# Optimization experiments

Measured on AMD Instinct MI355X. Metric: run time of the kernel, lower is better.

Reference implementation:

```python
import jax, jax.numpy as jnp
import numpy as np

R, N, E = 6, 50000, 200000
D, H, C, O = 768, 4, 64, 64  # input_dim, heads, hidden_dim1, output_dim


def _gatv2(x, src, tgt, Wl_r, Wr_r, att_r, b_r):
    # PyG GATv2Conv (concat=True, add_self_loops=True, negative_slope=0.2)
    n = x.shape[0]
    xl = (x @ Wl_r).reshape(n, H, C)  # source transform (lin_l)
    xr = (x @ Wr_r).reshape(n, H, C)  # target transform (lin_r)
    loops = jnp.arange(n, dtype=src.dtype)
    s = jnp.concatenate([src, loops])
    t = jnp.concatenate([tgt, loops])
    e = jax.nn.leaky_relu(xl[s] + xr[t], 0.2)          # [E+N, H, C]
    logits = jnp.einsum('ehc,hc->eh', e, att_r)         # [E+N, H]
    m = jax.ops.segment_max(logits, t, num_segments=n)  # softmax over incoming edges
    a = jnp.exp(logits - m[t])
    denom = jax.ops.segment_sum(a, t, num_segments=n)
    alpha = a / (denom[t] + 1e-16)
    msg = xl[s] * alpha[:, :, None]                     # [E+N, H, C]
    out = jax.ops.segment_sum(msg, t, num_segments=n)
    return out.reshape(n, H * C) + b_r


def _graphconv(x, src, tgt, W_rel, W_root, b):
    # PyG GraphConv (aggr='add'): lin_rel(sum_j x_j) + lin_root(x)
    agg = jax.ops.segment_sum(x[src], tgt, num_segments=x.shape[0])
    return agg @ W_rel + b + x @ W_root


def setup_inputs() -> dict:
    key = jax.random.key(0)
    ks = jax.random.split(key, 12)
    s = 0.05
    return {
        'x': jax.random.normal(ks[0], (N, D), jnp.float32),
        'edge_index': jax.random.randint(ks[1], (R, 2, E), 0, N, jnp.int32),
        'Wl': jax.random.normal(ks[2], (R, D, H * C), jnp.float32) * s,
        'Wr': jax.random.normal(ks[3], (R, D, H * C), jnp.float32) * s,
        'att': jax.random.normal(ks[4], (R, H, C), jnp.float32) * s,
        'b_gat': jax.random.normal(ks[5], (R, H * C), jnp.float32) * s,
        'W_rel1': jax.random.normal(ks[6], (R, H * C, C), jnp.float32) * s,
        'W_root1': jax.random.normal(ks[7], (R, H * C, C), jnp.float32) * s,
        'b1': jax.random.normal(ks[8], (R, C), jnp.float32) * s,
        'W_rel2': jax.random.normal(ks[9], (R, C, O), jnp.float32) * s,
        'W_root2': jax.random.normal(ks[10], (R, C, O), jnp.float32) * s,
        'b2': jax.random.normal(ks[11], (R, O), jnp.float32) * s,
    }


def reference(x, edge_index, Wl, Wr, att, b_gat, W_rel1, W_root1, b1, W_rel2, W_root2, b2):
    outs = []
    for r in range(R):  # fixed small set of structurally distinct relation towers
        src, tgt = edge_index[r, 0], edge_index[r, 1]
        h = _gatv2(x, src, tgt, Wl[r], Wr[r], att[r], b_gat[r])
        h = jax.nn.relu(h)
        h = jax.nn.relu(_graphconv(h, src, tgt, W_rel1[r], W_root1[r], b1[r]))
        h = _graphconv(h, src, tgt, W_rel2[r], W_root2[r], b2[r])
        outs.append(h)
    return jnp.stack(outs, axis=1)  # [N, R, O]
```

## Files before the change

kernel.cpp:

```cpp
#include <hip/hip_runtime.h>
#include <hip/hip_bf16.h>
#include <math.h>

#define RREL 6
#define NN   50000
#define EE   200000
#define DD   768
#define HH   4
#define CC   64
#define HC   256
#define OO   64
#define MPAD 50176
#define SCAN_B 49
#define NT   12

typedef __attribute__((ext_vector_type(8))) short short8;
typedef __attribute__((ext_vector_type(4))) float f32x4;
typedef __attribute__((ext_vector_type(8))) unsigned short ushort8v;
typedef __attribute__((ext_vector_type(4))) unsigned short ushort4v;

__device__ __forceinline__ float b2f(unsigned short u) {
  return __uint_as_float(((unsigned)u) << 16);
}
__device__ __forceinline__ unsigned short f2b(float f) {
  __hip_bfloat16 h = __float2bfloat16(f);
  unsigned short u;
  __builtin_memcpy(&u, &h, 2);
  return u;
}

__device__ __forceinline__ void gload16(const void* g, void* s) {
  typedef __attribute__((address_space(1))) void gvoid;
  typedef __attribute__((address_space(3))) void svoid;
  __builtin_amdgcn_global_load_lds((gvoid*)(unsigned long long)g,
                                   (svoid*)(unsigned long long)s, 16, 0, 0);
}

__global__ __launch_bounds__(256) void k_cvt_x(const float* __restrict__ x,
                                               unsigned short* __restrict__ xb) {
  long t = (long)blockIdx.x * 256 + threadIdx.x;
  long base = t * 8;
  int row = (int)(base / DD);
  ushort8v o;
  if (row < NN) {
    float4 a = *(const float4*)(x + base);
    float4 b = *(const float4*)(x + base + 4);
    o[0] = f2b(a.x); o[1] = f2b(a.y); o[2] = f2b(a.z); o[3] = f2b(a.w);
    o[4] = f2b(b.x); o[5] = f2b(b.y); o[6] = f2b(b.z); o[7] = f2b(b.w);
  } else {
    o = (ushort8v)0;
  }
  *(ushort8v*)(xb + base) = o;
}

__global__ __launch_bounds__(256) void k_repack_w(const float* __restrict__ Wl,
                                                  const float* __restrict__ Wr,
                                                  unsigned short* __restrict__ Wt) {
  __shared__ float t[32][33];
  int k0 = blockIdx.x * 32, j0 = blockIdx.y * 32, r = blockIdx.z;
  int tx = threadIdx.x & 31, ty = threadIdx.x >> 5;
#pragma unroll
  for (int s = 0; s < 4; s++) {
    int k = k0 + ty + 8 * s, j = j0 + tx;
    float v = (j < HC) ? Wl[((long)r * DD + k) * HC + j]
                       : Wr[((long)r * DD + k) * HC + (j - HC)];
    t[ty + 8 * s][tx] = v;
  }
  __syncthreads();
#pragma unroll
  for (int s = 0; s < 4; s++) {
    int j = j0 + ty + 8 * s, k = k0 + tx;
    Wt[((long)r * 512 + j) * DD + k] = f2b(t[tx][ty + 8 * s]);
  }
}

__global__ void k_repack_gc(const float* __restrict__ Wrel, const float* __restrict__ Wroot,
                            unsigned short* __restrict__ Bt, int K) {
  int idx = blockIdx.x * blockDim.x + threadIdx.x;
  if (idx >= RREL * 64 * K) return;
  int k = idx % K;
  int o = (idx / K) % 64;
  int r = idx / (64 * K);
  int h = K >> 1;
  float v = (k < h) ? Wrel[((long)r * h + k) * 64 + o]
                    : Wroot[((long)r * h + (k - h)) * 64 + o];
  Bt[idx] = f2b(v);
}

#define STAGE_A(HALF, TT)                                                              \
  if ((TT) < NT) {                                                                     \
    long ko = (long)(TT) * 128;                                                        \
    char* db = ldsA + (((TT) & 1) << 15);                                              \
    gload16(AgB + (long)((HALF) * 64 + rA) * 1536 + ko + xcol,                         \
            db + ((HALF) * 64) * 128 + wave * 1024);                                   \
    gload16(AgB + (long)((HALF) * 64 + 128 + rA) * 1536 + ko + xcol,                   \
            db + ((HALF) * 64 + 128) * 128 + wave * 1024);                             \
  }

#define STAGE_B(HALF, TT)                                                              \
  if ((TT) < NT) {                                                                     \
    long ko = (long)(TT) * 128;                                                        \
    char* db = ldsB + (((TT) & 1) << 15);                                              \
    gload16(BgB + (long)(rb0 + (HALF) * 32 + lane8) * 1536 + ko + xcol,                \
            db + (rb0 + (HALF) * 32) * 128);                                           \
    gload16(BgB + (long)(rb1 + (HALF) * 32 + lane8) * 1536 + ko + xcol,                \
            db + (rb1 + (HALF) * 32) * 128);                                           \
  }

#define MMQ(PA, AOFF, NH)                                                              \
  do {                                                                                 \
    _Pragma("unroll") for (int fi = 0; fi < 4; ++fi)                                   \
    _Pragma("unroll") for (int fj = 0; fj < 2; ++fj) {                                 \
      f32x4 c = acc[(AOFF) + fi][(NH) * 2 + fj];                                       \
      c = __builtin_amdgcn_mfma_f32_16x16x32_bf16(PA[fi][0], pb[NH][fj][0], c, 0, 0, 0);\
      c = __builtin_amdgcn_mfma_f32_16x16x32_bf16(PA[fi][1], pb[NH][fj][1], c, 0, 0, 0);\
      acc[(AOFF) + fi][(NH) * 2 + fj] = c;                                             \
    }                                                                                  \
  } while (0)

__global__ __launch_bounds__(512, 2) void k_gemm(const short* __restrict__ A,
                                                 const short* __restrict__ Bt,
                                                 unsigned short* __restrict__ Yall) {
  __shared__ __align__(16) char ldsA[65536];
  __shared__ __align__(16) char ldsB[65536];
  int tid = threadIdx.x;
  int wgid = blockIdx.x;
  int swz = (wgid & 7) * 294 + (wgid >> 3);
  int bm = swz / 12, bn = swz % 12;
  int lane = tid & 63, wave = tid >> 6;
  int warp_m = wave >> 2, warp_n = wave & 3;
  int wm = warp_m * 128, wn = warp_n * 64;
  int l16 = lane & 15, quad = lane >> 4;
  int gm0 = bm * 256;
  const char* AgB = (const char*)A + (long)gm0 * 1536;
  const char* BgB = (const char*)Bt + (long)bn * 256 * 1536;
  int rA = tid >> 3;
  int lane8 = lane >> 3;
  long xcol = (long)(((tid & 7) ^ (rA & 7)) * 16);
  int rb0 = (wave >> 2) * 64 + (wave & 3) * 8;
  int rb1 = rb0 + 128;
  int s0 = (quad ^ (l16 & 7)) * 16, s1 = s0 ^ 64;
  f32x4 acc[8][4] = {};

  STAGE_A(0, 0); STAGE_B(0, 0); STAGE_A(1, 0); STAGE_B(1, 0);
  STAGE_A(0, 1); STAGE_B(0, 1);
  asm volatile("s_waitcnt vmcnt(4)" ::: "memory");
  __builtin_amdgcn_s_barrier();

  for (int t = 0; t < NT; ++t) {
    int bo = (t & 1) << 15;
    const char* Ard = ldsA + bo + (wm + l16) * 128;
    const char* Brd = ldsB + bo + (wn + l16) * 128;
    short8 pa0[4][2], pa1[4][2], pb[2][2][2];
    STAGE_A(1, t + 1);
    STAGE_B(1, t + 1);
#pragma unroll
    for (int fi = 0; fi < 4; ++fi) {
      pa0[fi][0] = *(const short8*)(Ard + (fi * 16) * 128 + s0);
      pa0[fi][1] = *(const short8*)(Ard + (fi * 16) * 128 + s1);
    }
#pragma unroll
    for (int nh = 0; nh < 2; ++nh)
#pragma unroll
      for (int fj = 0; fj < 2; ++fj) {
        pb[nh][fj][0] = *(const short8*)(Brd + (nh * 32 + fj * 16) * 128 + s0);
        pb[nh][fj][1] = *(const short8*)(Brd + (nh * 32 + fj * 16) * 128 + s1);
      }
    __builtin_amdgcn_s_barrier();
    asm volatile("s_waitcnt lgkmcnt(0)" ::: "memory");
    __builtin_amdgcn_s_setprio(1);
    MMQ(pa0, 0, 0);
    __builtin_amdgcn_s_setprio(0);
#pragma unroll
    for (int fi = 0; fi < 4; ++fi) {
      pa1[fi][0] = *(const short8*)(Ard + ((64 + fi * 16)) * 128 + s0);
      pa1[fi][1] = *(const short8*)(Ard + ((64 + fi * 16)) * 128 + s1);
    }
    __builtin_amdgcn_s_setprio(1);
    MMQ(pa0, 0, 1);
    __builtin_amdgcn_s_setprio(0);
    __builtin_amdgcn_s_barrier();
    STAGE_A(0, t + 2);
    STAGE_B(0, t + 2);
    asm volatile("s_waitcnt lgkmcnt(0)" ::: "memory");
    __builtin_amdgcn_s_setprio(1);
    MMQ(pa1, 4, 0);
    MMQ(pa1, 4, 1);
    __builtin_amdgcn_s_setprio(0);
    if (t < NT - 2)       asm volatile("s_waitcnt vmcnt(4)" ::: "memory");
    else if (t == NT - 2) asm volatile("s_waitcnt vmcnt(0)" ::: "memory");
    __builtin_amdgcn_s_barrier();
  }

  int rel = bn >> 1;
  unsigned short* Yr = Yall + (long)rel * MPAD * 512;
  int cb = (bn & 1) * 256 + wn;
#pragma unroll
  for (int i = 0; i < 8; ++i) {
    int rowb = gm0 + wm + (i >> 2) * 64 + (i & 3) * 16 + quad * 4;
#pragma unroll
    for (int j = 0; j < 4; ++j) {
      int col = cb + (j >> 1) * 32 + (j & 1) * 16 + l16;
#pragma unroll
      for (int reg = 0; reg < 4; ++reg)
        Yr[(long)(rowb + reg) * 512 + col] = f2b(acc[i][j][reg]);
    }
  }
}

template <int K, bool RELU, bool OBF16>
__global__ __launch_bounds__(256) void k_gcgemm(const short* __restrict__ Aall,
                                                const short* __restrict__ Btall,
                                                const float* __restrict__ biasall,
                                                void* __restrict__ outp, long ldo, int ocol,
                                                long orelstride) {
  __shared__ __align__(16) short As[128 * 32];
  __shared__ __align__(16) short Bs[64 * 32];
  int tid = threadIdx.x;
  int bm = blockIdx.x, r = blockIdx.y;
  const short* A  = Aall + (long)r * MPAD * K;
  const short* Bt = Btall + (long)r * 64 * K;
  const float* bias = biasall + (long)r * 64;
  int lane = tid & 63, wave = tid >> 6;
  int quad = lane >> 4, l16 = lane & 15;
  f32x4 acc[2][4] = {};
  const short* Ag = A + (long)bm * 128 * K;
  int lr = lane >> 2, lc = (lane & 3) * 8;
  const short* ga0 = Ag + (long)(wave * 16 + lr) * K + lc;
  const short* ga1 = Ag + (long)(64 + wave * 16 + lr) * K + lc;
  const short* gb0 = Bt + (long)(wave * 16 + lr) * K + lc;
  short* la0 = &As[(wave * 16) * 32];
  short* la1 = &As[(64 + wave * 16) * 32];
  short* lb0 = &Bs[(wave * 16) * 32];
  for (int k0 = 0; k0 < K; k0 += 32) {
    gload16(ga0 + k0, la0);
    gload16(ga1 + k0, la1);
    gload16(gb0 + k0, lb0);
    __syncthreads();
    short8 af[2], bf[4];
#pragma unroll
    for (int i = 0; i < 2; i++) af[i] = *(const short8*)&As[(wave * 32 + i * 16 + l16) * 32 + quad * 8];
#pragma unroll
    for (int j = 0; j < 4; j++) bf[j] = *(const short8*)&Bs[(j * 16 + l16) * 32 + quad * 8];
#pragma unroll
    for (int i = 0; i < 2; i++)
#pragma unroll
      for (int j = 0; j < 4; j++)
        acc[i][j] = __builtin_amdgcn_mfma_f32_16x16x32_bf16(af[i], bf[j], acc[i][j], 0, 0, 0);
    __syncthreads();
  }
#pragma unroll
  for (int i = 0; i < 2; i++)
#pragma unroll
    for (int j = 0; j < 4; j++)
#pragma unroll
      for (int reg = 0; reg < 4; reg++) {
        int row = bm * 128 + wave * 32 + i * 16 + quad * 4 + reg;
        int col = j * 16 + l16;
        float v = acc[i][j][reg] + bias[col];
        if (RELU) v = fmaxf(v, 0.f);
        if (OBF16) {
          ((unsigned short*)outp)[(long)r * orelstride + (long)row * ldo + ocol + col] = f2b(v);
        } else {
          if (row < NN) ((float*)outp)[(long)r * orelstride + (long)row * ldo + ocol + col] = v;
        }
      }
}

__global__ void k_deg6(const int* __restrict__ ei, int* __restrict__ deg6) {
  long e = (long)blockIdx.x * blockDim.x + threadIdx.x;
  if (e >= (long)RREL * EE) return;
  int r = e / EE, i = e % EE;
  int t = ei[(long)r * 2 * EE + EE + i];
  atomicAdd(&deg6[(long)r * NN + t], 1);
}

__global__ __launch_bounds__(256) void k_bsum(const int* __restrict__ deg6, int* __restrict__ bsum) {
  int r = blockIdx.y, b = blockIdx.x, tid = threadIdx.x;
  const int* deg = deg6 + (long)r * NN;
  int i0 = b * 1024 + tid * 4;
  int s = 0;
#pragma unroll
  for (int j = 0; j < 4; j++) { int i = i0 + j; if (i < NN) s += deg[i]; }
#pragma unroll
  for (int m = 1; m < 64; m <<= 1) s += __shfl_xor(s, m);
  __shared__ int ws[4];
  if ((tid & 63) == 0) ws[tid >> 6] = s;
  __syncthreads();
  if (tid == 0) bsum[r * SCAN_B + b] = ws[0] + ws[1] + ws[2] + ws[3];
}

__global__ void k_bscan(int* __restrict__ bsum) {
  int w = threadIdx.x >> 6, l = threadIdx.x & 63;
  int v = (l < SCAN_B) ? bsum[w * SCAN_B + l] : 0;
  int incl = v;
#pragma unroll
  for (int d = 1; d < 64; d <<= 1) { int t = __shfl_up(incl, d); if (l >= d) incl += t; }
  if (l < SCAN_B) bsum[w * SCAN_B + l] = incl - v;
}

__global__ __launch_bounds__(256) void k_boff(const int* __restrict__ deg6, const int* __restrict__ bsum,
                                              int* __restrict__ off6, int* __restrict__ cur6) {
  int r = blockIdx.y, b = blockIdx.x, tid = threadIdx.x;
  const int* deg = deg6 + (long)r * NN;
  int i0 = b * 1024 + tid * 4;
  int v[4], s = 0;
#pragma unroll
  for (int j = 0; j < 4; j++) { int i = i0 + j; v[j] = (i < NN) ? deg[i] : 0; s += v[j]; }
  int l = tid & 63, wv = tid >> 6;
  int incl = s;
#pragma unroll
  for (int d = 1; d < 64; d <<= 1) { int t = __shfl_up(incl, d); if (l >= d) incl += t; }
  __shared__ int ws[4];
  if (l == 63) ws[wv] = incl;
  __syncthreads();
  int pre = incl - s;
  for (int k = 0; k < wv; k++) pre += ws[k];
  pre += bsum[r * SCAN_B + b];
  int e0 = pre;
#pragma unroll
  for (int j = 0; j < 4; j++) {
    int i = i0 + j;
    if (i < NN) { off6[(long)r * NN + i] = e0; cur6[(long)r * NN + i] = e0; }
    e0 += v[j];
  }
}

__global__ void k_scatter6(const int* __restrict__ ei, int* __restrict__ cur6,
                           int* __restrict__ ssrc6) {
  long e = (long)blockIdx.x * blockDim.x + threadIdx.x;
  if (e >= (long)RREL * EE) return;
  int r = e / EE, i = e % EE;
  int src = ei[(long)r * 2 * EE + i];
  int t   = ei[(long)r * 2 * EE + EE + i];
  int p = atomicAdd(&cur6[(long)r * NN + t], 1);
  ssrc6[(long)r * EE + p] = src;
}

__global__ __launch_bounds__(256) void k_gat(unsigned short* __restrict__ Yall,
                                             const int* __restrict__ ssrc6,
                                             const int* __restrict__ off6, const int* __restrict__ deg6,
                                             const float* __restrict__ attall,
                                             const float* __restrict__ bgall) {
  int r = blockIdx.y;
  unsigned short* Y = Yall + (long)r * MPAD * 512;
  const int* ssrc = ssrc6 + (long)r * EE;
  const float* att = attall + r * HC;
  const float* bg  = bgall + r * HC;
  int l = threadIdx.x & 63;
  int n = blockIdx.x * 4 + (threadIdx.x >> 6);
  if (n >= NN) return;
  const unsigned short* yb = Y + (long)n * 512;
  ushort4v xlv = *(const ushort4v*)(yb + 4 * l);
  ushort4v xrv = *(const ushort4v*)(yb + 256 + 4 * l);
  float xl[4], xr[4];
#pragma unroll
  for (int j = 0; j < 4; j++) { xl[j] = b2f(xlv[j]); xr[j] = b2f(xrv[j]); }
  float4 at4 = *(const float4*)(att + 4 * l);
  float at[4] = {at4.x, at4.y, at4.z, at4.w};
  float num[4] = {0.f, 0.f, 0.f, 0.f}, den = 0.f;
  {
    float lg = 0.f;
#pragma unroll
    for (int j = 0; j < 4; j++) {
      float e = xl[j] + xr[j];
      e = e > 0.f ? e : 0.2f * e;
      lg += at[j] * e;
    }
    lg += __shfl_xor(lg, 1); lg += __shfl_xor(lg, 2);
    lg += __shfl_xor(lg, 4); lg += __shfl_xor(lg, 8);
    float a = expf(lg);
    den += a;
#pragma unroll
    for (int j = 0; j < 4; j++) num[j] += a * xl[j];
  }
  int st = off6[(long)r * NN + n], cnt = deg6[(long)r * NN + n];
  int i = 0;
  for (; i + 2 <= cnt; i += 2) {
    int s0 = ssrc[st + i], s1 = ssrc[st + i + 1];
    ushort4v v0 = *(const ushort4v*)(Y + (long)s0 * 512 + 4 * l);
    ushort4v v1 = *(const ushort4v*)(Y + (long)s1 * 512 + 4 * l);
    float x0[4], x1[4];
#pragma unroll
    for (int j = 0; j < 4; j++) { x0[j] = b2f(v0[j]); x1[j] = b2f(v1[j]); }
    float lg0 = 0.f, lg1 = 0.f;
#pragma unroll
    for (int j = 0; j < 4; j++) {
      float e0 = x0[j] + xr[j]; e0 = e0 > 0.f ? e0 : 0.2f * e0; lg0 += at[j] * e0;
      float e1 = x1[j] + xr[j]; e1 = e1 > 0.f ? e1 : 0.2f * e1; lg1 += at[j] * e1;
    }
    lg0 += __shfl_xor(lg0, 1); lg1 += __shfl_xor(lg1, 1);
    lg0 += __shfl_xor(lg0, 2); lg1 += __shfl_xor(lg1, 2);
    lg0 += __shfl_xor(lg0, 4); lg1 += __shfl_xor(lg1, 4);
    lg0 += __shfl_xor(lg0, 8); lg1 += __shfl_xor(lg1, 8);
    float a0 = expf(lg0), a1 = expf(lg1);
    den += a0 + a1;
#pragma unroll
    for (int j = 0; j < 4; j++) num[j] += a0 * x0[j] + a1 * x1[j];
  }
  if (i < cnt) {
    int s0 = ssrc[st + i];
    ushort4v v0 = *(const ushort4v*)(Y + (long)s0 * 512 + 4 * l);
    float x0[4];
#pragma unroll
    for (int j = 0; j < 4; j++) x0[j] = b2f(v0[j]);
    float lg = 0.f;
#pragma unroll
    for (int j = 0; j < 4; j++) {
      float e = x0[j] + xr[j];
      e = e > 0.f ? e : 0.2f * e;
      lg += at[j] * e;
    }
    lg += __shfl_xor(lg, 1); lg += __shfl_xor(lg, 2);
    lg += __shfl_xor(lg, 4); lg += __shfl_xor(lg, 8);
    float a = expf(lg);
    den += a;
#pragma unroll
    for (int j = 0; j < 4; j++) num[j] += a * x0[j];
  }
  float4 bg4 = *(const float4*)(bg + 4 * l);
  float bgj[4] = {bg4.x, bg4.y, bg4.z, bg4.w};
  ushort4v o;
  float inv = 1.f / (den + 1e-16f);
#pragma unroll
  for (int j = 0; j < 4; j++) o[j] = f2b(fmaxf(num[j] * inv + bgj[j], 0.f));
  *(ushort4v*)(Y + (long)n * 512 + 256 + 4 * l) = o;
}

__global__ __launch_bounds__(256) void k_agg1(unsigned short* __restrict__ Yall,
                                              const int* __restrict__ ssrc6,
                                              const int* __restrict__ off6,
                                              const int* __restrict__ deg6) {
  int r = blockIdx.y;
  unsigned short* Y = Yall + (long)r * MPAD * 512;
  const int* ssrc = ssrc6 + (long)r * EE;
  int l = threadIdx.x & 63;
  int n = blockIdx.x * 4 + (threadIdx.x >> 6);
  if (n >= NN) return;
  float acc[4] = {0.f, 0.f, 0.f, 0.f};
  int st = off6[(long)r * NN + n], cnt = deg6[(long)r * NN + n];
  int i = 0;
  for (; i + 4 <= cnt; i += 4) {
    int s0 = ssrc[st + i], s1 = ssrc[st + i + 1], s2 = ssrc[st + i + 2], s3 = ssrc[st + i + 3];
    ushort4v v0 = *(const ushort4v*)(Y + (long)s0 * 512 + 256 + 4 * l);
    ushort4v v1 = *(const ushort4v*)(Y + (long)s1 * 512 + 256 + 4 * l);
    ushort4v v2 = *(const ushort4v*)(Y + (long)s2 * 512 + 256 + 4 * l);
    ushort4v v3 = *(const ushort4v*)(Y + (long)s3 * 512 + 256 + 4 * l);
#pragma unroll
    for (int j = 0; j < 4; j++)
      acc[j] += b2f(v0[j]) + b2f(v1[j]) + b2f(v2[j]) + b2f(v3[j]);
  }
  for (; i < cnt; i++) {
    int s = ssrc[st + i];
    ushort4v v = *(const ushort4v*)(Y + (long)s * 512 + 256 + 4 * l);
#pragma unroll
    for (int j = 0; j < 4; j++) acc[j] += b2f(v[j]);
  }
  ushort4v o;
#pragma unroll
  for (int j = 0; j < 4; j++) o[j] = f2b(acc[j]);
  *(ushort4v*)(Y + (long)n * 512 + 4 * l) = o;
}

__global__ __launch_bounds__(256) void k_agg2(unsigned short* __restrict__ ABall,
                                              const int* __restrict__ ssrc6,
                                              const int* __restrict__ off6,
                                              const int* __restrict__ deg6) {
  int r = blockIdx.y;
  unsigned short* AB2 = ABall + (long)r * MPAD * 128;
  const int* ssrc = ssrc6 + (long)r * EE;
  int l = threadIdx.x & 63;
  int n = blockIdx.x * 4 + (threadIdx.x >> 6);
  if (n >= NN) return;
  float acc = 0.f;
  int st = off6[(long)r * NN + n], cnt = deg6[(long)r * NN + n];
  int i = 0;
  for (; i + 4 <= cnt; i += 4) {
    int s0 = ssrc[st + i], s1 = ssrc[st + i + 1], s2 = ssrc[st + i + 2], s3 = ssrc[st + i + 3];
    acc += b2f(AB2[(long)s0 * 128 + OO + l]) + b2f(AB2[(long)s1 * 128 + OO + l]) +
           b2f(AB2[(long)s2 * 128 + OO + l]) + b2f(AB2[(long)s3 * 128 + OO + l]);
  }
  for (; i < cnt; i++) {
    int s = ssrc[st + i];
    acc += b2f(AB2[(long)s * 128 + OO + l]);
  }
  AB2[(long)n * 128 + l] = f2b(acc);
}

extern "C" void kernel_launch(void* const* d_in, const int* in_sizes, int n_in,
                              void* d_out, int out_size, void* d_ws, size_t ws_size,
                              hipStream_t stream) {
  (void)in_sizes; (void)n_in; (void)out_size;
  const float* x      = (const float*)d_in[0];
  const int*   ei     = (const int*)d_in[1];
  const float* Wl     = (const float*)d_in[2];
  const float* Wr     = (const float*)d_in[3];
  const float* att    = (const float*)d_in[4];
  const float* bg     = (const float*)d_in[5];
  const float* Wrel1  = (const float*)d_in[6];
  const float* Wroot1 = (const float*)d_in[7];
  const float* b1     = (const float*)d_in[8];
  const float* Wrel2  = (const float*)d_in[9];
  const float* Wroot2 = (const float*)d_in[10];
  const float* b2     = (const float*)d_in[11];
  float* out = (float*)d_out;

  char* ws = (char*)d_ws;
  size_t ofs = 0;
  auto alloc = [&](size_t bytes) {
    char* p = ws + ofs;
    ofs += (bytes + 255) & ~(size_t)255;
    return p;
  };
  unsigned short* Xb   = (unsigned short*)alloc((size_t)MPAD * DD * 2);
  unsigned short* Wt   = (unsigned short*)alloc((size_t)RREL * 512 * DD * 2);
  unsigned short* Wt1  = (unsigned short*)alloc((size_t)RREL * 64 * 512 * 2);
  unsigned short* Wt2  = (unsigned short*)alloc((size_t)RREL * 64 * 128 * 2);
  unsigned short* Yall = (unsigned short*)alloc((size_t)RREL * MPAD * 512 * 2);
  unsigned short* AB2  = (unsigned short*)alloc((size_t)RREL * MPAD * 128 * 2);
  int* deg6   = (int*)alloc((size_t)RREL * NN * 4);
  int* off6   = (int*)alloc((size_t)RREL * NN * 4);
  int* cur6   = (int*)alloc((size_t)RREL * NN * 4);
  int* bsum   = (int*)alloc((size_t)RREL * SCAN_B * 4);
  int* ssrc6  = (int*)alloc((size_t)RREL * EE * 4);
  if (ofs > ws_size) return;

  k_cvt_x<<<(int)((long)MPAD * DD / 8 / 256), 256, 0, stream>>>(x, Xb);
  k_repack_w<<<dim3(DD / 32, 512 / 32, RREL), 256, 0, stream>>>(Wl, Wr, Wt);
  k_repack_gc<<<(RREL * 64 * 512 + 255) / 256, 256, 0, stream>>>(Wrel1, Wroot1, Wt1, 512);
  k_repack_gc<<<(RREL * 64 * 128 + 255) / 256, 256, 0, stream>>>(Wrel2, Wroot2, Wt2, 128);
  hipMemsetAsync(deg6, 0, (size_t)RREL * NN * 4, stream);
  k_deg6<<<((long)RREL * EE + 255) / 256, 256, 0, stream>>>(ei, deg6);
  k_bsum<<<dim3(SCAN_B, RREL), 256, 0, stream>>>(deg6, bsum);
  k_bscan<<<1, 384, 0, stream>>>(bsum);
  k_boff<<<dim3(SCAN_B, RREL), 256, 0, stream>>>(deg6, bsum, off6, cur6);
  k_scatter6<<<((long)RREL * EE + 255) / 256, 256, 0, stream>>>(ei, cur6, ssrc6);

  k_gemm<<<dim3(196 * 12), 512, 0, stream>>>((const short*)Xb, (const short*)Wt, Yall);
  k_gat<<<dim3(NN / 4, RREL), 256, 0, stream>>>(Yall, ssrc6, off6, deg6, att, bg);
  k_agg1<<<dim3(NN / 4, RREL), 256, 0, stream>>>(Yall, ssrc6, off6, deg6);
  k_gcgemm<512, true, true><<<dim3(MPAD / 128, RREL), 256, 0, stream>>>(
      (const short*)Yall, (const short*)Wt1, b1, (void*)AB2, 128, OO, (long)MPAD * 128);
  k_agg2<<<dim3(NN / 4, RREL), 256, 0, stream>>>(AB2, ssrc6, off6, deg6);
  k_gcgemm<128, false, false><<<dim3(MPAD / 128, RREL), 256, 0, stream>>>(
      (const short*)AB2, (const short*)Wt2, b2, (void*)out, RREL * OO, 0, 64);
}
```

Before: 1.210 ms.

## Transform node features before aggregation in GraphConv layers

Reorders each GraphConv so the linear maps are applied first (Z = h·Wrel, R = h·Wroot in one GEMM), and neighbours are then summed over the 64-wide Z instead of the 256-wide h. This removes the separate 256-channel gather (agg1) and halves the GEMM K dimension. Bias, root term and ReLU move into the aggregation kernels. The cost is an extra bf16 rounding of Z before summation, which changes the numerics slightly.

```diff
diff --git a/kernel.cpp b/kernel.cpp
--- a/kernel.cpp
+++ b/kernel.cpp
@@ -74,16 +74,15 @@
   }
 }
 
-__global__ void k_repack_gc(const float* __restrict__ Wrel, const float* __restrict__ Wroot,
+__global__ void k_repack_zr(const float* __restrict__ Wrel, const float* __restrict__ Wroot,
                             unsigned short* __restrict__ Bt, int K) {
   int idx = blockIdx.x * blockDim.x + threadIdx.x;
-  if (idx >= RREL * 64 * K) return;
+  if (idx >= RREL * 128 * K) return;
   int k = idx % K;
-  int o = (idx / K) % 64;
-  int r = idx / (64 * K);
-  int h = K >> 1;
-  float v = (k < h) ? Wrel[((long)r * h + k) * 64 + o]
-                    : Wroot[((long)r * h + (k - h)) * 64 + o];
+  int j = (idx / K) % 128;
+  int r = idx / (128 * K);
+  float v = (j < 64) ? Wrel[((long)r * K + k) * 64 + j]
+                     : Wroot[((long)r * K + k) * 64 + (j - 64)];
   Bt[idx] = f2b(v);
 }
 
@@ -208,62 +207,58 @@
   }
 }
 
-template <int K, bool RELU, bool OBF16>
-__global__ __launch_bounds__(256) void k_gcgemm(const short* __restrict__ Aall,
-                                                const short* __restrict__ Btall,
-                                                const float* __restrict__ biasall,
-                                                void* __restrict__ outp, long ldo, int ocol,
-                                                long orelstride) {
+template <int K>
+__global__ __launch_bounds__(256) void k_zr(const unsigned short* __restrict__ Abase,
+                                            long lda, long aoff,
+                                            const unsigned short* __restrict__ Btall,
+                                            unsigned short* __restrict__ ZRall) {
   __shared__ __align__(16) short As[128 * 32];
-  __shared__ __align__(16) short Bs[64 * 32];
+  __shared__ __align__(16) short Bs[128 * 32];
   int tid = threadIdx.x;
   int bm = blockIdx.x, r = blockIdx.y;
-  const short* A  = Aall + (long)r * MPAD * K;
-  const short* Bt = Btall + (long)r * 64 * K;
-  const float* bias = biasall + (long)r * 64;
+  const unsigned short* A  = Abase + (long)r * MPAD * lda + aoff;
+  const unsigned short* Bt = Btall + (long)r * 128 * K;
+  unsigned short* ZR = ZRall + (long)r * MPAD * 128;
   int lane = tid & 63, wave = tid >> 6;
   int quad = lane >> 4, l16 = lane & 15;
-  f32x4 acc[2][4] = {};
-  const short* Ag = A + (long)bm * 128 * K;
+  f32x4 acc[2][8] = {};
+  const unsigned short* Ag = A + (long)bm * 128 * lda;
   int lr = lane >> 2, lc = (lane & 3) * 8;
-  const short* ga0 = Ag + (long)(wave * 16 + lr) * K + lc;
-  const short* ga1 = Ag + (long)(64 + wave * 16 + lr) * K + lc;
-  const short* gb0 = Bt + (long)(wave * 16 + lr) * K + lc;
+  const unsigned short* ga0 = Ag + (long)(wave * 16 + lr) * lda + lc;
+  const unsigned short* ga1 = Ag + (long)(64 + wave * 16 + lr) * lda + lc;
+  const unsigned short* gb0 = Bt + (long)(wave * 16 + lr) * K + lc;
+  const unsigned short* gb1 = Bt + (long)(64 + wave * 16 + lr) * K + lc;
   short* la0 = &As[(wave * 16) * 32];
   short* la1 = &As[(64 + wave * 16) * 32];
   short* lb0 = &Bs[(wave * 16) * 32];
+  short* lb1 = &Bs[(64 + wave * 16) * 32];
   for (int k0 = 0; k0 < K; k0 += 32) {
     gload16(ga0 + k0, la0);
     gload16(ga1 + k0, la1);
     gload16(gb0 + k0, lb0);
+    gload16(gb1 + k0, lb1);
     __syncthreads();
-    short8 af[2], bf[4];
+    short8 af[2], bf[8];
 #pragma unroll
     for (int i = 0; i < 2; i++) af[i] = *(const short8*)&As[(wave * 32 + i * 16 + l16) * 32 + quad * 8];
 #pragma unroll
-    for (int j = 0; j < 4; j++) bf[j] = *(const short8*)&Bs[(j * 16 + l16) * 32 + quad * 8];
+    for (int j = 0; j < 8; j++) bf[j] = *(const short8*)&Bs[(j * 16 + l16) * 32 + quad * 8];
 #pragma unroll
     for (int i = 0; i < 2; i++)
 #pragma unroll
-      for (int j = 0; j < 4; j++)
+      for (int j = 0; j < 8; j++)
         acc[i][j] = __builtin_amdgcn_mfma_f32_16x16x32_bf16(af[i], bf[j], acc[i][j], 0, 0, 0);
     __syncthreads();
   }
 #pragma unroll
   for (int i = 0; i < 2; i++)
 #pragma unroll
-    for (int j = 0; j < 4; j++)
+    for (int j = 0; j < 8; j++)
 #pragma unroll
       for (int reg = 0; reg < 4; reg++) {
         int row = bm * 128 + wave * 32 + i * 16 + quad * 4 + reg;
         int col = j * 16 + l16;
-        float v = acc[i][j][reg] + bias[col];
-        if (RELU) v = fmaxf(v, 0.f);
-        if (OBF16) {
-          ((unsigned short*)outp)[(long)r * orelstride + (long)row * ldo + ocol + col] = f2b(v);
-        } else {
-          if (row < NN) ((float*)outp)[(long)r * orelstride + (long)row * ldo + ocol + col] = v;
-        }
+        ZR[(long)row * 128 + col] = f2b(acc[i][j][reg]);
       }
 }
 
@@ -427,47 +422,15 @@
   *(ushort4v*)(Y + (long)n * 512 + 256 + 4 * l) = o;
 }
 
-__global__ __launch_bounds__(256) void k_agg1(unsigned short* __restrict__ Yall,
-                                              const int* __restrict__ ssrc6,
-                                              const int* __restrict__ off6,
-                                              const int* __restrict__ deg6) {
+__global__ __launch_bounds__(256) void k_aggc1(const unsigned short* __restrict__ ZRall,
+                                               unsigned short* __restrict__ Yall,
+                                               const int* __restrict__ ssrc6,
+                                               const int* __restrict__ off6,
+                                               const int* __restrict__ deg6,
+                                               const float* __restrict__ b1all) {
   int r = blockIdx.y;
+  const unsigned short* ZR = ZRall + (long)r * MPAD * 128;
   unsigned short* Y = Yall + (long)r * MPAD * 512;
-  const int* ssrc = ssrc6 + (long)r * EE;
-  int l = threadIdx.x & 63;
-  int n = blockIdx.x * 4 + (threadIdx.x >> 6);
-  if (n >= NN) return;
-  float acc[4] = {0.f, 0.f, 0.f, 0.f};
-  int st = off6[(long)r * NN + n], cnt = deg6[(long)r * NN + n];
-  int i = 0;
-  for (; i + 4 <= cnt; i += 4) {
-    int s0 = ssrc[st + i], s1 = ssrc[st + i + 1], s2 = ssrc[st + i + 2], s3 = ssrc[st + i + 3];
-    ushort4v v0 = *(const ushort4v*)(Y + (long)s0 * 512 + 256 + 4 * l);
-    ushort4v v1 = *(const ushort4v*)(Y + (long)s1 * 512 + 256 + 4 * l);
-    ushort4v v2 = *(const ushort4v*)(Y + (long)s2 * 512 + 256 + 4 * l);
-    ushort4v v3 = *(const ushort4v*)(Y + (long)s3 * 512 + 256 + 4 * l);
-#pragma unroll
-    for (int j = 0; j < 4; j++)
-      acc[j] += b2f(v0[j]) + b2f(v1[j]) + b2f(v2[j]) + b2f(v3[j]);
-  }
-  for (; i < cnt; i++) {
-    int s = ssrc[st + i];
-    ushort4v v = *(const ushort4v*)(Y + (long)s * 512 + 256 + 4 * l);
-#pragma unroll
-    for (int j = 0; j < 4; j++) acc[j] += b2f(v[j]);
-  }
-  ushort4v o;
-#pragma unroll
-  for (int j = 0; j < 4; j++) o[j] = f2b(acc[j]);
-  *(ushort4v*)(Y + (long)n * 512 + 4 * l) = o;
-}
-
-__global__ __launch_bounds__(256) void k_agg2(unsigned short* __restrict__ ABall,
-                                              const int* __restrict__ ssrc6,
-                                              const int* __restrict__ off6,
-                                              const int* __restrict__ deg6) {
-  int r = blockIdx.y;
-  unsigned short* AB2 = ABall + (long)r * MPAD * 128;
   const int* ssrc = ssrc6 + (long)r * EE;
   int l = threadIdx.x & 63;
   int n = blockIdx.x * 4 + (threadIdx.x >> 6);
@@ -477,14 +440,43 @@
   int i = 0;
   for (; i + 4 <= cnt; i += 4) {
     int s0 = ssrc[st + i], s1 = ssrc[st + i + 1], s2 = ssrc[st + i + 2], s3 = ssrc[st + i + 3];
-    acc += b2f(AB2[(long)s0 * 128 + OO + l]) + b2f(AB2[(long)s1 * 128 + OO + l]) +
-           b2f(AB2[(long)s2 * 128 + OO + l]) + b2f(AB2[(long)s3 * 128 + OO + l]);
+    acc += b2f(ZR[(long)s0 * 128 + l]) + b2f(ZR[(long)s1 * 128 + l]) +
+           b2f(ZR[(long)s2 * 128 + l]) + b2f(ZR[(long)s3 * 128 + l]);
   }
   for (; i < cnt; i++) {
     int s = ssrc[st + i];
-    acc += b2f(AB2[(long)s * 128 + OO + l]);
-  }
-  AB2[(long)n * 128 + l] = f2b(acc);
+    acc += b2f(ZR[(long)s * 128 + l]);
+  }
+  float v = acc + b2f(ZR[(long)n * 128 + 64 + l]) + b1all[r * 64 + l];
+  Y[(long)n * 512 + l] = f2b(fmaxf(v, 0.f));
+}
+
+__global__ __launch_bounds__(256) void k_aggc2(const unsigned short* __restrict__ ZRall,
+                                               float* __restrict__ out,
+                                               const int* __restrict__ ssrc6,
+                                               const int* __restrict__ off6,
+                                               const int* __restrict__ deg6,
+                                               const float* __restrict__ b2all) {
+  int r = blockIdx.y;
+  const unsigned short* ZR = ZRall + (long)r * MPAD * 128;
+  const int* ssrc = ssrc6 + (long)r * EE;
+  int l = threadIdx.x & 63;
+  int n = blockIdx.x * 4 + (threadIdx.x >> 6);
+  if (n >= NN) return;
+  float acc = 0.f;
+  int st = off6[(long)r * NN + n], cnt = deg6[(long)r * NN + n];
+  int i = 0;
+  for (; i + 4 <= cnt; i += 4) {
+    int s0 = ssrc[st + i], s1 = ssrc[st + i + 1], s2 = ssrc[st + i + 2], s3 = ssrc[st + i + 3];
+    acc += b2f(ZR[(long)s0 * 128 + l]) + b2f(ZR[(long)s1 * 128 + l]) +
+           b2f(ZR[(long)s2 * 128 + l]) + b2f(ZR[(long)s3 * 128 + l]);
+  }
+  for (; i < cnt; i++) {
+    int s = ssrc[st + i];
+    acc += b2f(ZR[(long)s * 128 + l]);
+  }
+  float v = acc + b2f(ZR[(long)n * 128 + 64 + l]) + b2all[r * 64 + l];
+  out[(long)n * (RREL * 64) + r * 64 + l] = v;
 }
 
 extern "C" void kernel_launch(void* const* d_in, const int* in_sizes, int n_in,
@@ -514,10 +506,10 @@
   };
   unsigned short* Xb   = (unsigned short*)alloc((size_t)MPAD * DD * 2);
   unsigned short* Wt   = (unsigned short*)alloc((size_t)RREL * 512 * DD * 2);
-  unsigned short* Wt1  = (unsigned short*)alloc((size_t)RREL * 64 * 512 * 2);
-  unsigned short* Wt2  = (unsigned short*)alloc((size_t)RREL * 64 * 128 * 2);
+  unsigned short* Bt1  = (unsigned short*)alloc((size_t)RREL * 128 * 256 * 2);
+  unsigned short* Bt2  = (unsigned short*)alloc((size_t)RREL * 128 * 64 * 2);
   unsigned short* Yall = (unsigned short*)alloc((size_t)RREL * MPAD * 512 * 2);
-  unsigned short* AB2  = (unsigned short*)alloc((size_t)RREL * MPAD * 128 * 2);
+  unsigned short* ZR   = (unsigned short*)alloc((size_t)RREL * MPAD * 128 * 2);
   int* deg6   = (int*)alloc((size_t)RREL * NN * 4);
   int* off6   = (int*)alloc((size_t)RREL * NN * 4);
   int* cur6   = (int*)alloc((size_t)RREL * NN * 4);
@@ -527,8 +519,8 @@
 
   k_cvt_x<<<(int)((long)MPAD * DD / 8 / 256), 256, 0, stream>>>(x, Xb);
   k_repack_w<<<dim3(DD / 32, 512 / 32, RREL), 256, 0, stream>>>(Wl, Wr, Wt);
-  k_repack_gc<<<(RREL * 64 * 512 + 255) / 256, 256, 0, stream>>>(Wrel1, Wroot1, Wt1, 512);
-  k_repack_gc<<<(RREL * 64 * 128 + 255) / 256, 256, 0, stream>>>(Wrel2, Wroot2, Wt2, 128);
+  k_repack_zr<<<(RREL * 128 * 256 + 255) / 256, 256, 0, stream>>>(Wrel1, Wroot1, Bt1, 256);
+  k_repack_zr<<<(RREL * 128 * 64 + 255) / 256, 256, 0, stream>>>(Wrel2, Wroot2, Bt2, 64);
   hipMemsetAsync(deg6, 0, (size_t)RREL * NN * 4, stream);
   k_deg6<<<((long)RREL * EE + 255) / 256, 256, 0, stream>>>(ei, deg6);
   k_bsum<<<dim3(SCAN_B, RREL), 256, 0, stream>>>(deg6, bsum);
@@ -538,10 +530,8 @@
 
   k_gemm<<<dim3(196 * 12), 512, 0, stream>>>((const short*)Xb, (const short*)Wt, Yall);
   k_gat<<<dim3(NN / 4, RREL), 256, 0, stream>>>(Yall, ssrc6, off6, deg6, att, bg);
-  k_agg1<<<dim3(NN / 4, RREL), 256, 0, stream>>>(Yall, ssrc6, off6, deg6);
-  k_gcgemm<512, true, true><<<dim3(MPAD / 128, RREL), 256, 0, stream>>>(
-      (const short*)Yall, (const short*)Wt1, b1, (void*)AB2, 128, OO, (long)MPAD * 128);
-  k_agg2<<<dim3(NN / 4, RREL), 256, 0, stream>>>(AB2, ssrc6, off6, deg6);
-  k_gcgemm<128, false, false><<<dim3(MPAD / 128, RREL), 256, 0, stream>>>(
-      (const short*)AB2, (const short*)Wt2, b2, (void*)out, RREL * OO, 0, 64);
-}
+  k_zr<256><<<dim3(MPAD / 128, RREL), 256, 0, stream>>>(Yall, 512, 256, Bt1, ZR);
+  k_aggc1<<<dim3(NN / 4, RREL), 256, 0, stream>>>(ZR, Yall, ssrc6, off6, deg6, b1);
+  k_zr<64><<<dim3(MPAD / 128, RREL), 256, 0, stream>>>(Yall, 512, 0, Bt2, ZR);
+  k_aggc2<<<dim3(NN / 4, RREL), 256, 0, stream>>>(ZR, out, ssrc6, off6, deg6, b2);
+}
```

Result: faster. 1.142 ms (-5.6%).
